# Performance work log

Hardware: AMD Instinct MI355X
Metric: run time of the kernel (lower is better)

The kernel has to match this reference:

```python
import jax, jax.numpy as jnp
import numpy as np

B, N, C, H, K = 16, 1024, 384, 6, 8
HID = int(C * 2.0)  # mlp_ratio = 2.0
HD = C // H


def _layernorm(x, w, b, eps=1e-5):
    m = x.mean(-1, keepdims=True)
    v = ((x - m) ** 2).mean(-1, keepdims=True)
    return (x - m) * jax.lax.rsqrt(v + eps) * w + b


def setup_inputs() -> dict:
    key = jax.random.key(0)
    ks = jax.random.split(key, 16)
    x = jax.random.normal(ks[0], (B, N, C), jnp.float32)
    # knn indices within each batch, offset by batch*N (as in get_knn_index)
    idx = jax.random.randint(ks[1], (B, K, N), 0, N)
    base = jnp.arange(B, dtype=jnp.int32)[:, None, None] * N
    knn_index = (idx + base).reshape(-1).astype(jnp.int32)
    s = 0.02
    p = {
        "x": x,
        "knn_index": knn_index,
        "ln1_w": jnp.ones((C,), jnp.float32),
        "ln1_b": jnp.zeros((C,), jnp.float32),
        "w_qkv": jax.random.normal(ks[2], (C, 3 * C), jnp.float32) * s,  # qkv_bias=False
        "w_proj": jax.random.normal(ks[3], (C, C), jnp.float32) * s,
        "b_proj": jnp.zeros((C,), jnp.float32),
        "w_knn": jax.random.normal(ks[4], (2 * C, C), jnp.float32) * s,
        "b_knn": jnp.zeros((C,), jnp.float32),
        "w_merge": jax.random.normal(ks[5], (2 * C, C), jnp.float32) * s,
        "b_merge": jnp.zeros((C,), jnp.float32),
        "ln2_w": jnp.ones((C,), jnp.float32),
        "ln2_b": jnp.zeros((C,), jnp.float32),
        "w_fc1": jax.random.normal(ks[6], (C, HID), jnp.float32) * s,
        "b_fc1": jnp.zeros((HID,), jnp.float32),
        "w_fc2": jax.random.normal(ks[7], (HID, C), jnp.float32) * s,
        "b_fc2": jnp.zeros((C,), jnp.float32),
    }
    return p


def reference(x, knn_index, ln1_w, ln1_b, w_qkv, w_proj, b_proj, w_knn, b_knn,
              w_merge, b_merge, ln2_w, ln2_b, w_fc1, b_fc1, w_fc2, b_fc2):
    nx = _layernorm(x, ln1_w, ln1_b)  # [B,N,C]

    # --- self attention ---
    qkv = (nx @ w_qkv).reshape(B, N, 3, H, HD)
    q, k, v = qkv[:, :, 0], qkv[:, :, 1], qkv[:, :, 2]  # [B,N,H,HD]
    scale = HD ** (-0.5)
    attn = jnp.einsum("bnhd,bmhd->bhnm", q, k) * scale
    attn = jax.nn.softmax(attn, axis=-1)
    a_out = jnp.einsum("bhnm,bmhd->bnhd", attn, v).reshape(B, N, C)
    x1 = a_out @ w_proj + b_proj

    # --- graph feature: gather, relative concat, Linear+LeakyReLU, max over k ---
    feat = nx.reshape(B * N, C)[knn_index].reshape(B, K, N, C)
    center = nx[:, None, :, :]  # [B,1,N,C]
    g = jnp.concatenate([feat - center, jnp.broadcast_to(center, (B, K, N, C))], axis=-1)
    knn_f = jax.nn.leaky_relu(g @ w_knn + b_knn, negative_slope=0.2)
    knn_f = knn_f.max(axis=1)  # [B,N,C]

    x1 = jnp.concatenate([x1, knn_f], axis=-1) @ w_merge + b_merge
    x = x + x1

    # --- MLP ---
    h = _layernorm(x, ln2_w, ln2_b)
    h = jax.nn.gelu(h @ w_fc1 + b_fc1, approximate=False) @ w_fc2 + b_fc2
    return x + h
```

## Files before the change

### kernel.cpp

```cpp
#include <hip/hip_runtime.h>
#include <hip/hip_bf16.h>
#include <math.h>

#define BN_ROWS 16384
#define CDIM 384
#define NH 6
#define BBATCH 16
#define NNN 1024

typedef unsigned short u16;
typedef unsigned int u32;
typedef __attribute__((ext_vector_type(8))) short short8;
typedef __attribute__((ext_vector_type(4))) float floatx4;

__device__ __forceinline__ float b2f(u16 s) { return __uint_as_float(((u32)s) << 16); }
__device__ __forceinline__ u16 f2b(float f) {
    __hip_bfloat16 h = __float2bfloat16(f);
    u16 s; __builtin_memcpy(&s, &h, 2); return s;
}
__device__ __forceinline__ u32 cvt_pk_bf16(float lo, float hi) {
    u32 r;
    asm("v_cvt_pk_bf16_f32 %0, %1, %2" : "=v"(r) : "v"(lo), "v"(hi));
    return r;
}
__device__ __forceinline__ void gload_lds16(const u16* g, u16* l) {
    __builtin_amdgcn_global_load_lds(
        (const __attribute__((address_space(1))) unsigned int*)g,
        (__attribute__((address_space(3))) unsigned int*)l, 16, 0, 0);
}

__global__ __launch_bounds__(256) void pack_all(
    const float* __restrict__ W0, u16* __restrict__ T0,
    const float* __restrict__ W1, u16* __restrict__ T1,
    const float* __restrict__ W2, u16* __restrict__ T2,
    const float* __restrict__ W3, u16* __restrict__ T3,
    const float* __restrict__ W4, u16* __restrict__ T4,
    const float* __restrict__ W5, u16* __restrict__ T5)
{
    const float* W; u16* T; int K, N;
    switch (blockIdx.z) {
        case 0: W = W0; T = T0; K = 384; N = 1152; break;
        case 1: W = W1; T = T1; K = 384; N = 384;  break;
        case 2: W = W2; T = T2; K = 768; N = 384;  break;
        case 3: W = W3; T = T3; K = 768; N = 384;  break;
        case 4: W = W4; T = T4; K = 384; N = 768;  break;
        default: W = W5; T = T5; K = 768; N = 384; break;
    }
    const int n0 = blockIdx.x * 32, k0 = blockIdx.y * 32;
    if (n0 >= N || k0 >= K) return;
    __shared__ float s[32][33];
    const int tx = threadIdx.x & 31, ty = threadIdx.x >> 5;
#pragma unroll
    for (int i = 0; i < 4; ++i)
        s[ty + 8 * i][tx] = W[(size_t)(k0 + ty + 8 * i) * N + n0 + tx];
    __syncthreads();
#pragma unroll
    for (int i = 0; i < 4; ++i)
        T[(size_t)(n0 + ty + 8 * i) * K + k0 + tx] = f2b(s[tx][ty + 8 * i]);
}

__global__ __launch_bounds__(64) void ln_kernel(const float* __restrict__ xin,
                                                const float* __restrict__ w,
                                                const float* __restrict__ b,
                                                u16* __restrict__ out)
{
    const int row = blockIdx.x;
    const int t = threadIdx.x;
    const size_t base = (size_t)row * CDIM;
    float v[6];
#pragma unroll
    for (int i = 0; i < 6; ++i) v[i] = xin[base + t + 64 * i];
    float s = 0.f, s2 = 0.f;
#pragma unroll
    for (int i = 0; i < 6; ++i) { s += v[i]; s2 += v[i] * v[i]; }
#pragma unroll
    for (int m = 1; m < 64; m <<= 1) {
        s  += __shfl_xor(s,  m, 64);
        s2 += __shfl_xor(s2, m, 64);
    }
    const float mean = s * (1.0f / CDIM);
    const float var  = s2 * (1.0f / CDIM) - mean * mean;
    const float rs   = rsqrtf(var + 1e-5f);
#pragma unroll
    for (int i = 0; i < 6; ++i) {
        int c = t + 64 * i;
        out[base + c] = f2b((v[i] - mean) * rs * w[c] + b[c]);
    }
}

template<int ACT, bool HAS_BIAS, bool HAS_RES, bool OUT_F32, int MODE, int NT, bool SWZ>
__global__ __launch_bounds__(256) void gemm_mfma_kernel(
    const u16* __restrict__ A, int lda,
    const u16* __restrict__ Bt, const u16* __restrict__ Bt2, int ldbt,
    u16* Cb, u16* Cb2, float* Cf, int ldc,
    const float* __restrict__ bias,
    const float* res,
    int K)
{
    constexpr int NTL = NT / 32;
    __shared__ u16 As[3][128 * 32];
    __shared__ u16 Bs[3][NT * 32];
    const int tid  = threadIdx.x;
    const int wv   = tid >> 6;
    const int lane = tid & 63;
    const int l15  = lane & 15;
    const int quad = lane >> 4;

    int m0, n0;
    if (SWZ) {
        const int nbx = gridDim.x;
        const int total = nbx * gridDim.y;
        int lin = blockIdx.x + nbx * blockIdx.y;
        const int cpx = total >> 3;
        lin = (lin & 7) * cpx + (lin >> 3);
        m0 = (lin / nbx) * 128;
        n0 = (lin % nbx) * NT;
    } else {
        m0 = blockIdx.y * 128;
        n0 = blockIdx.x * NT;
    }

    const int woffm = (wv >> 1) * 64;
    const int woffn = (wv & 1) * (NT / 2);

    const u16* bsrc = (MODE == 2 && n0 >= 384) ? Bt2 : Bt;
    const int  bn0  = (MODE == 2 && n0 >= 384) ? (n0 - 384) : n0;

    floatx4 acc[4][NTL];
#pragma unroll
    for (int mt = 0; mt < 4; ++mt)
#pragma unroll
        for (int nt = 0; nt < NTL; ++nt) acc[mt][nt] = (floatx4){0.f, 0.f, 0.f, 0.f};

    const int gsw  = 8 * ((lane & 3) ^ ((lane >> 3) & 3));
    const int rloc = lane >> 2;
    const int rdsw = 8 * (quad ^ ((l15 >> 1) & 3));

    auto stage = [&](int kt, int p) {
#pragma unroll
        for (int j = 0; j < 2; ++j) {
            const int slab = 32 * wv + 16 * j;
            gload_lds16(A + (size_t)(m0 + slab + rloc) * lda + kt + gsw, &As[p][slab * 32]);
        }
        if (NT == 128) {
#pragma unroll
            for (int j = 0; j < 2; ++j) {
                const int slab = 32 * wv + 16 * j;
                gload_lds16(bsrc + (size_t)(bn0 + slab + rloc) * ldbt + kt + gsw, &Bs[p][slab * 32]);
            }
        } else {
            const int slab = 16 * wv;
            gload_lds16(bsrc + (size_t)(bn0 + slab + rloc) * ldbt + kt + gsw, &Bs[p][slab * 32]);
        }
    };

    stage(0, 0);
    if (32 < K) stage(32, 1);
    int s = 0;
    for (int kt = 0; kt < K; kt += 32, ++s) {
        if (kt + 32 < K) {
            if constexpr (NT == 128) asm volatile("s_waitcnt vmcnt(4)" ::: "memory");
            else                     asm volatile("s_waitcnt vmcnt(3)" ::: "memory");
        } else {
            asm volatile("s_waitcnt vmcnt(0)" ::: "memory");
        }
        __builtin_amdgcn_sched_barrier(0);
        __builtin_amdgcn_s_barrier();
        __builtin_amdgcn_sched_barrier(0);

        const u16* Ac = As[s % 3];
        const u16* Bc = Bs[s % 3];
        short8 af[4], bf[NTL];
#pragma unroll
        for (int mt = 0; mt < 4; ++mt)
            af[mt] = *(const short8*)(Ac + (woffm + mt * 16 + l15) * 32 + rdsw);
#pragma unroll
        for (int nt = 0; nt < NTL; ++nt)
            bf[nt] = *(const short8*)(Bc + (woffn + nt * 16 + l15) * 32 + rdsw);
#pragma unroll
        for (int mt = 0; mt < 4; ++mt)
#pragma unroll
            for (int nt = 0; nt < NTL; ++nt)
                acc[mt][nt] = __builtin_amdgcn_mfma_f32_16x16x32_bf16(
                    bf[nt], af[mt], acc[mt][nt], 0, 0, 0);
        if (kt + 64 < K) stage(kt + 64, (s + 2) % 3);
    }

#pragma unroll
    for (int mt = 0; mt < 4; ++mt) {
        const int gr = m0 + woffm + mt * 16 + l15;
#pragma unroll
        for (int nt = 0; nt < NTL; ++nt) {
            const int gc0 = n0 + woffn + nt * 16 + quad * 4;
            float v4[4];
#pragma unroll
            for (int rr = 0; rr < 4; ++rr) v4[rr] = acc[mt][nt][rr];
            if (HAS_BIAS) {
                const floatx4 bv = *(const floatx4*)(bias + gc0);
#pragma unroll
                for (int rr = 0; rr < 4; ++rr) v4[rr] += bv[rr];
            }
            if (MODE == 2) {
                if (gc0 >= 384) {
                    const floatx4 bv = *(const floatx4*)(bias + gc0 - 384);
#pragma unroll
                    for (int rr = 0; rr < 4; ++rr) v4[rr] += bv[rr];
                }
            }
            if (ACT == 1) {
#pragma unroll
                for (int rr = 0; rr < 4; ++rr)
                    v4[rr] = 0.5f * v4[rr] * (1.0f + erff(v4[rr] * 0.70710678118654752f));
            }
            if (HAS_RES) {
                const floatx4 rv = *(const floatx4*)(res + (size_t)gr * ldc + gc0);
#pragma unroll
                for (int rr = 0; rr < 4; ++rr) v4[rr] += rv[rr];
            }
            if (MODE == 1) {
                const int t3  = gc0 / 384;
                const int rem = gc0 - t3 * 384;
                const int hh = rem >> 6, dd = rem & 63;
                const int bb = gr >> 10, nn = gr & 1023;
                u32 lo = cvt_pk_bf16(v4[0], v4[1]);
                u32 hi = cvt_pk_bf16(v4[2], v4[3]);
                *(uint2*)(Cb + ((size_t)((bb * 6 + hh) * 1024 + nn)) * 192 + t3 * 64 + dd) =
                    make_uint2(lo, hi);
            } else if (MODE == 2) {
                u32 lo = cvt_pk_bf16(v4[0], v4[1]);
                u32 hi = cvt_pk_bf16(v4[2], v4[3]);
                if (gc0 < 384)
                    *(uint2*)(Cb  + (size_t)gr * 384 + gc0)       = make_uint2(lo, hi);
                else
                    *(uint2*)(Cb2 + (size_t)gr * 384 + gc0 - 384) = make_uint2(lo, hi);
            } else if (OUT_F32) {
                floatx4 vv = {v4[0], v4[1], v4[2], v4[3]};
                *(floatx4*)(Cf + (size_t)gr * ldc + gc0) = vv;
            } else {
                u32 lo = cvt_pk_bf16(v4[0], v4[1]);
                u32 hi = cvt_pk_bf16(v4[2], v4[3]);
                *(uint2*)(Cb + (size_t)gr * ldc + gc0) = make_uint2(lo, hi);
            }
        }
    }
}

__global__ __launch_bounds__(256) void attn_mfma_kernel(const u16* __restrict__ qkv2,
                                                        u16* __restrict__ aout)
{
    const int id = blockIdx.x;
    const int rxcd = id & 7;
    const int j = id >> 3;
    const int slab = rxcd + 8 * (j % 12);
    const int qtile = j / 12;
    const int b = slab / NH, h = slab % NH;

    const int wave = threadIdx.x >> 6;
    const int lane = threadIdx.x & 63;
    const int l15 = lane & 15;
    const int quad = lane >> 4;
    const int qbase = qtile * 128 + wave * 32;
    const int tid = threadIdx.x;

    const u16* slabp = qkv2 + ((size_t)(b * NH + h) << 10) * 192;

    __shared__ __align__(16) u16 Ks[64 * 72];
    __shared__ __align__(16) u16 Vt[64 * 72];
    __shared__ __align__(16) u16 Ps[4][32 * 72];

    short8 qf[2][2];
#pragma unroll
    for (int nt = 0; nt < 2; ++nt) {
        const u16* qrow = slabp + (size_t)(qbase + nt * 16 + l15) * 192;
        qf[nt][0] = *(const short8*)(qrow + quad * 8);
        qf[nt][1] = *(const short8*)(qrow + 32 + quad * 8);
    }

    short8 vones;
#pragma unroll
    for (int i = 0; i < 8; ++i) vones[i] = (l15 == 0) ? (short)0x3F80 : (short)0;

    floatx4 Oacc[2][4];
    floatx4 rAcc[2];
#pragma unroll
    for (int mt = 0; mt < 2; ++mt) {
        rAcc[mt] = (floatx4){0.f, 0.f, 0.f, 0.f};
#pragma unroll
        for (int nt = 0; nt < 4; ++nt) Oacc[mt][nt] = (floatx4){0.f, 0.f, 0.f, 0.f};
    }

    const int key = tid >> 2, dblk = (tid & 3) * 16;
    const int kp2 = tid & 31, db = (tid >> 5) * 8;
    uint4 kr0, kr1, vr0, vr1;
    {
        const u16* kp = slabp + (size_t)key * 192 + 64 + dblk;
        kr0 = *(const uint4*)(kp);
        kr1 = *(const uint4*)(kp + 8);
        const u16* vp = slabp + (size_t)(2 * kp2) * 192 + 128 + db;
        vr0 = *(const uint4*)(vp);
        vr1 = *(const uint4*)(vp + 192);
    }

    for (int kc = 0; kc < NNN; kc += 64) {
        *(uint4*)(Ks + key * 72 + dblk)     = kr0;
        *(uint4*)(Ks + key * 72 + dblk + 8) = kr1;
        {
            u32 a0[4] = {vr0.x, vr0.y, vr0.z, vr0.w};
            u32 a1[4] = {vr1.x, vr1.y, vr1.z, vr1.w};
#pragma unroll
            for (int i = 0; i < 4; ++i) {
                u32 lo = __builtin_amdgcn_perm(a1[i], a0[i], 0x05040100u);
                u32 hi = __builtin_amdgcn_perm(a1[i], a0[i], 0x07060302u);
                *(u32*)(Vt + (size_t)(db + 2 * i)     * 72 + 2 * kp2) = lo;
                *(u32*)(Vt + (size_t)(db + 2 * i + 1) * 72 + 2 * kp2) = hi;
            }
        }
        __syncthreads();

        if (kc + 64 < NNN) {
            const u16* kp = slabp + (size_t)(kc + 64 + key) * 192 + 64 + dblk;
            kr0 = *(const uint4*)(kp);
            kr1 = *(const uint4*)(kp + 8);
            const u16* vp = slabp + (size_t)(kc + 64 + 2 * kp2) * 192 + 128 + db;
            vr0 = *(const uint4*)(vp);
            vr1 = *(const uint4*)(vp + 192);
        }

        floatx4 sc[4][2];
        __builtin_amdgcn_s_setprio(1);
#pragma unroll
        for (int kt_ = 0; kt_ < 4; ++kt_) {
            short8 kf0 = *(const short8*)(Ks + (kt_ * 16 + l15) * 72 + quad * 8);
            short8 kf1 = *(const short8*)(Ks + (kt_ * 16 + l15) * 72 + 32 + quad * 8);
#pragma unroll
            for (int nt = 0; nt < 2; ++nt) {
                floatx4 s = {0.f, 0.f, 0.f, 0.f};
                s = __builtin_amdgcn_mfma_f32_16x16x32_bf16(kf0, qf[nt][0], s, 0, 0, 0);
                s = __builtin_amdgcn_mfma_f32_16x16x32_bf16(kf1, qf[nt][1], s, 0, 0, 0);
                sc[kt_][nt] = s;
            }
        }
        __builtin_amdgcn_s_setprio(0);

#pragma unroll
        for (int kt_ = 0; kt_ < 4; ++kt_)
#pragma unroll
            for (int nt = 0; nt < 2; ++nt) {
                float pv[4];
#pragma unroll
                for (int rr = 0; rr < 4; ++rr)
                    pv[rr] = __expf(sc[kt_][nt][rr] * 0.125f);
                u32 lo = cvt_pk_bf16(pv[0], pv[1]);
                u32 hi = cvt_pk_bf16(pv[2], pv[3]);
                *(uint2*)(Ps[wave] + (nt * 16 + l15) * 72 + kt_ * 16 + quad * 4) =
                    make_uint2(lo, hi);
            }

        short8 pf[2][2];
#pragma unroll
        for (int mt = 0; mt < 2; ++mt) {
            pf[mt][0] = *(const short8*)(Ps[wave] + (mt * 16 + l15) * 72 + quad * 8);
            pf[mt][1] = *(const short8*)(Ps[wave] + (mt * 16 + l15) * 72 + 32 + quad * 8);
        }
        __builtin_amdgcn_s_setprio(1);
#pragma unroll
        for (int mt = 0; mt < 2; ++mt) {
            rAcc[mt] = __builtin_amdgcn_mfma_f32_16x16x32_bf16(pf[mt][0], vones, rAcc[mt], 0, 0, 0);
            rAcc[mt] = __builtin_amdgcn_mfma_f32_16x16x32_bf16(pf[mt][1], vones, rAcc[mt], 0, 0, 0);
        }
#pragma unroll
        for (int nt = 0; nt < 4; ++nt) {
#pragma unroll
            for (int kk = 0; kk < 2; ++kk) {
                short8 vf = *(const short8*)(Vt + (size_t)(nt * 16 + l15) * 72 + kk * 32 + quad * 8);
#pragma unroll
                for (int mt = 0; mt < 2; ++mt)
                    Oacc[mt][nt] = __builtin_amdgcn_mfma_f32_16x16x32_bf16(
                        pf[mt][kk], vf, Oacc[mt][nt], 0, 0, 0);
            }
        }
        __builtin_amdgcn_s_setprio(0);
        __syncthreads();
    }

#pragma unroll
    for (int mt = 0; mt < 2; ++mt) {
#pragma unroll
        for (int rr = 0; rr < 4; ++rr) {
            float l = __shfl(rAcc[mt][rr], quad << 4, 64);
            float inv = 1.0f / l;
            int q = qbase + mt * 16 + quad * 4 + rr;
#pragma unroll
            for (int nt = 0; nt < 4; ++nt)
                aout[(size_t)(b * NNN + q) * CDIM + h * 64 + nt * 16 + l15] =
                    f2b(Oacc[mt][nt][rr] * inv);
        }
    }
}

__global__ __launch_bounds__(128) void knnmax_kernel(const u16* __restrict__ t1,
                                                     const u16* __restrict__ t2,
                                                     const int* __restrict__ idx,
                                                     u16* __restrict__ x1cat)
{
    const int bn = blockIdx.x * 2 + (threadIdx.x >> 6);
    const int lane = threadIdx.x & 63;
    if (lane >= 48) return;
    const int b = bn >> 10, n = bn & 1023;
    int ind[8];
#pragma unroll
    for (int k = 0; k < 8; ++k) ind[k] = idx[b * 8192 + k * 1024 + n];
    const int c0 = lane * 8;
    const size_t rbase = (size_t)bn * CDIM + c0;
    short8 v1 = *(const short8*)(t1 + rbase);
    short8 v2 = *(const short8*)(t2 + rbase);
    float basef[8], mx[8];
#pragma unroll
    for (int j = 0; j < 8; ++j) {
        basef[j] = b2f((u16)v2[j]) - b2f((u16)v1[j]);
        mx[j] = -1e30f;
    }
#pragma unroll
    for (int k = 0; k < 8; ++k) {
        short8 nv = *(const short8*)(t1 + (size_t)ind[k] * CDIM + c0);
#pragma unroll
        for (int j = 0; j < 8; ++j) {
            float v = b2f((u16)nv[j]) + basef[j];
            v = (v > 0.f) ? v : 0.2f * v;
            mx[j] = fmaxf(mx[j], v);
        }
    }
    short8 ov;
#pragma unroll
    for (int j = 0; j < 8; ++j) ov[j] = (short)f2b(mx[j]);
    *(short8*)(x1cat + (size_t)bn * 768 + CDIM + c0) = ov;
}

extern "C" void kernel_launch(void* const* d_in, const int* in_sizes, int n_in,
                              void* d_out, int out_size, void* d_ws, size_t ws_size,
                              hipStream_t stream)
{
    (void)in_sizes; (void)n_in; (void)out_size; (void)ws_size;
    const float* x     = (const float*)d_in[0];
    const int*   knn   = (const int*)d_in[1];
    const float* ln1w  = (const float*)d_in[2];
    const float* ln1b  = (const float*)d_in[3];
    const float* wqkv  = (const float*)d_in[4];
    const float* wproj = (const float*)d_in[5];
    const float* bproj = (const float*)d_in[6];
    const float* wknn  = (const float*)d_in[7];
    const float* bknn  = (const float*)d_in[8];
    const float* wmrg  = (const float*)d_in[9];
    const float* bmrg  = (const float*)d_in[10];
    const float* ln2w  = (const float*)d_in[11];
    const float* ln2b  = (const float*)d_in[12];
    const float* wfc1  = (const float*)d_in[13];
    const float* bfc1  = (const float*)d_in[14];
    const float* wfc2  = (const float*)d_in[15];
    const float* bfc2  = (const float*)d_in[16];

    u16* wsb = (u16*)d_ws;
    const size_t RE = (size_t)BN_ROWS * CDIM;
    u16* nxb   = wsb;
    u16* qkvb  = wsb + RE;
    u16* x1cat = wsb + RE;
    u16* t1b   = wsb + 3 * RE;
    u16* hinb  = wsb;
    u16* h1b   = wsb + RE;
    u16* wqkvT  = wsb + 4 * RE;
    u16* wprojT = wqkvT + 442368;
    u16* wknnT  = wprojT + 147456;
    u16* wmrgT  = wknnT + 294912;
    u16* wfc1T  = wmrgT + 294912;
    u16* wfc2T  = wfc1T + 294912;
    u16*   aoutb = (u16*)d_out;
    u16*   t2b   = (u16*)d_out;
    float* xmid  = (float*)d_out;

    pack_all<<<dim3(36, 24, 6), 256, 0, stream>>>(
        wqkv, wqkvT, wproj, wprojT, wknn, wknnT, wmrg, wmrgT, wfc1, wfc1T, wfc2, wfc2T);
    ln_kernel<<<BN_ROWS, 64, 0, stream>>>(x, ln1w, ln1b, nxb);
    gemm_mfma_kernel<0, false, false, false, 1, 128, true><<<dim3(9, 128), 256, 0, stream>>>(
        nxb, CDIM, wqkvT, nullptr, CDIM, qkvb, nullptr, nullptr, 0, nullptr, nullptr, CDIM);
    attn_mfma_kernel<<<768, 256, 0, stream>>>(qkvb, aoutb);
    gemm_mfma_kernel<0, true, false, false, 0, 64, true><<<dim3(6, 128), 256, 0, stream>>>(
        aoutb, CDIM, wprojT, nullptr, CDIM, x1cat, nullptr, nullptr, 768, bproj, nullptr, CDIM);
    gemm_mfma_kernel<0, false, false, false, 2, 128, true><<<dim3(6, 128), 256, 0, stream>>>(
        nxb, CDIM, wknnT, wknnT + 384, 768, t1b, t2b, nullptr, CDIM, bknn, nullptr, CDIM);
    knnmax_kernel<<<BN_ROWS / 2, 128, 0, stream>>>(t1b, t2b, knn, x1cat);
    gemm_mfma_kernel<0, true, true, true, 0, 64, true><<<dim3(6, 128), 256, 0, stream>>>(
        x1cat, 768, wmrgT, nullptr, 768, nullptr, nullptr, xmid, CDIM, bmrg, x, 768);
    ln_kernel<<<BN_ROWS, 64, 0, stream>>>(xmid, ln2w, ln2b, hinb);
    gemm_mfma_kernel<1, true, false, false, 0, 128, true><<<dim3(6, 128), 256, 0, stream>>>(
        hinb, CDIM, wfc1T, nullptr, CDIM, h1b, nullptr, nullptr, 768, bfc1, nullptr, CDIM);
    gemm_mfma_kernel<0, true, true, true, 0, 64, true><<<dim3(6, 128), 256, 0, stream>>>(
        h1b, 768, wfc2T, nullptr, 768, nullptr, nullptr, (float*)d_out, CDIM, bfc2, xmid, 768);
}
```

Before: 309.4 us.

## Fuse QKV and KNN projection GEMMs into one launch with double-buffered LDS

Adds a MODE 3 path to the GEMM so the QKV projection and both halves of the KNN linear run as one wider launch over nx (15 column tiles). This removes a kernel launch and reads nx once instead of twice. The GEMM pipeline also drops from triple to double buffering, with an extra barrier per k-step, which cuts LDS use but shortens prefetch depth. Workspace buffers are moved so t1/t2 live in the output buffer and aout in the workspace.

```diff
diff --git a/kernel.cpp b/kernel.cpp
--- a/kernel.cpp
+++ b/kernel.cpp
@@ -92,14 +92,14 @@
 __global__ __launch_bounds__(256) void gemm_mfma_kernel(
     const u16* __restrict__ A, int lda,
     const u16* __restrict__ Bt, const u16* __restrict__ Bt2, int ldbt,
-    u16* Cb, u16* Cb2, float* Cf, int ldc,
+    u16* Cb, u16* Cb2, u16* Cb3, float* Cf, int ldc,
     const float* __restrict__ bias,
     const float* res,
     int K)
 {
     constexpr int NTL = NT / 32;
-    __shared__ u16 As[3][128 * 32];
-    __shared__ u16 Bs[3][NT * 32];
+    __shared__ u16 As[2][128 * 32];
+    __shared__ u16 Bs[2][NT * 32];
     const int tid  = threadIdx.x;
     const int wv   = tid >> 6;
     const int lane = tid & 63;
@@ -123,8 +123,16 @@
     const int woffm = (wv >> 1) * 64;
     const int woffn = (wv & 1) * (NT / 2);
 
-    const u16* bsrc = (MODE == 2 && n0 >= 384) ? Bt2 : Bt;
-    const int  bn0  = (MODE == 2 && n0 >= 384) ? (n0 - 384) : n0;
+    const u16* bsrc; int brow0, koff, bld;
+    if constexpr (MODE == 3) {
+        if (n0 < 1152)      { bsrc = Bt;  brow0 = n0;        koff = 0;   bld = 384; }
+        else if (n0 < 1536) { bsrc = Bt2; brow0 = n0 - 1152; koff = 0;   bld = 768; }
+        else                { bsrc = Bt2; brow0 = n0 - 1536; koff = 384; bld = 768; }
+    } else {
+        bsrc  = (MODE == 2 && n0 >= 384) ? Bt2 : Bt;
+        brow0 = (MODE == 2 && n0 >= 384) ? (n0 - 384) : n0;
+        koff = 0; bld = ldbt;
+    }
 
     floatx4 acc[4][NTL];
 #pragma unroll
@@ -146,18 +154,20 @@
 #pragma unroll
             for (int j = 0; j < 2; ++j) {
                 const int slab = 32 * wv + 16 * j;
-                gload_lds16(bsrc + (size_t)(bn0 + slab + rloc) * ldbt + kt + gsw, &Bs[p][slab * 32]);
+                gload_lds16(bsrc + (size_t)(brow0 + slab + rloc) * bld + koff + kt + gsw,
+                            &Bs[p][slab * 32]);
             }
         } else {
             const int slab = 16 * wv;
-            gload_lds16(bsrc + (size_t)(bn0 + slab + rloc) * ldbt + kt + gsw, &Bs[p][slab * 32]);
+            gload_lds16(bsrc + (size_t)(brow0 + slab + rloc) * bld + koff + kt + gsw,
+                        &Bs[p][slab * 32]);
         }
     };
 
     stage(0, 0);
-    if (32 < K) stage(32, 1);
-    int s = 0;
-    for (int kt = 0; kt < K; kt += 32, ++s) {
+    stage(32, 1);
+    int cur = 0;
+    for (int kt = 0; kt < K; kt += 32) {
         if (kt + 32 < K) {
             if constexpr (NT == 128) asm volatile("s_waitcnt vmcnt(4)" ::: "memory");
             else                     asm volatile("s_waitcnt vmcnt(3)" ::: "memory");
@@ -168,22 +178,24 @@
         __builtin_amdgcn_s_barrier();
         __builtin_amdgcn_sched_barrier(0);
 
-        const u16* Ac = As[s % 3];
-        const u16* Bc = Bs[s % 3];
         short8 af[4], bf[NTL];
 #pragma unroll
         for (int mt = 0; mt < 4; ++mt)
-            af[mt] = *(const short8*)(Ac + (woffm + mt * 16 + l15) * 32 + rdsw);
+            af[mt] = *(const short8*)(As[cur] + (woffm + mt * 16 + l15) * 32 + rdsw);
 #pragma unroll
         for (int nt = 0; nt < NTL; ++nt)
-            bf[nt] = *(const short8*)(Bc + (woffn + nt * 16 + l15) * 32 + rdsw);
+            bf[nt] = *(const short8*)(Bs[cur] + (woffn + nt * 16 + l15) * 32 + rdsw);
 #pragma unroll
         for (int mt = 0; mt < 4; ++mt)
 #pragma unroll
             for (int nt = 0; nt < NTL; ++nt)
                 acc[mt][nt] = __builtin_amdgcn_mfma_f32_16x16x32_bf16(
                     bf[nt], af[mt], acc[mt][nt], 0, 0, 0);
-        if (kt + 64 < K) stage(kt + 64, (s + 2) % 3);
+        __builtin_amdgcn_sched_barrier(0);
+        __builtin_amdgcn_s_barrier();
+        __builtin_amdgcn_sched_barrier(0);
+        if (kt + 64 < K) stage(kt + 64, cur);
+        cur ^= 1;
     }
 
 #pragma unroll
@@ -200,12 +212,15 @@
 #pragma unroll
                 for (int rr = 0; rr < 4; ++rr) v4[rr] += bv[rr];
             }
-            if (MODE == 2) {
-                if (gc0 >= 384) {
-                    const floatx4 bv = *(const floatx4*)(bias + gc0 - 384);
-#pragma unroll
-                    for (int rr = 0; rr < 4; ++rr) v4[rr] += bv[rr];
-                }
+            if (MODE == 2 && gc0 >= 384) {
+                const floatx4 bv = *(const floatx4*)(bias + gc0 - 384);
+#pragma unroll
+                for (int rr = 0; rr < 4; ++rr) v4[rr] += bv[rr];
+            }
+            if (MODE == 3 && gc0 >= 1536) {
+                const floatx4 bv = *(const floatx4*)(bias + gc0 - 1536);
+#pragma unroll
+                for (int rr = 0; rr < 4; ++rr) v4[rr] += bv[rr];
             }
             if (ACT == 1) {
 #pragma unroll
@@ -217,7 +232,7 @@
 #pragma unroll
                 for (int rr = 0; rr < 4; ++rr) v4[rr] += rv[rr];
             }
-            if (MODE == 1) {
+            if (MODE == 1 || (MODE == 3 && gc0 < 1152)) {
                 const int t3  = gc0 / 384;
                 const int rem = gc0 - t3 * 384;
                 const int hh = rem >> 6, dd = rem & 63;
@@ -226,6 +241,13 @@
                 u32 hi = cvt_pk_bf16(v4[2], v4[3]);
                 *(uint2*)(Cb + ((size_t)((bb * 6 + hh) * 1024 + nn)) * 192 + t3 * 64 + dd) =
                     make_uint2(lo, hi);
+            } else if (MODE == 3) {
+                u32 lo = cvt_pk_bf16(v4[0], v4[1]);
+                u32 hi = cvt_pk_bf16(v4[2], v4[3]);
+                if (gc0 < 1536)
+                    *(uint2*)(Cb2 + (size_t)gr * 384 + gc0 - 1152) = make_uint2(lo, hi);
+                else
+                    *(uint2*)(Cb3 + (size_t)gr * 384 + gc0 - 1536) = make_uint2(lo, hi);
             } else if (MODE == 2) {
                 u32 lo = cvt_pk_bf16(v4[0], v4[1]);
                 u32 hi = cvt_pk_bf16(v4[2], v4[3]);
@@ -463,36 +485,34 @@
     const size_t RE = (size_t)BN_ROWS * CDIM;
     u16* nxb   = wsb;
     u16* qkvb  = wsb + RE;
+    u16* aoutb = wsb;
     u16* x1cat = wsb + RE;
-    u16* t1b   = wsb + 3 * RE;
     u16* hinb  = wsb;
     u16* h1b   = wsb + RE;
+    u16* t1b   = (u16*)d_out;
+    u16* t2b   = (u16*)d_out + RE;
+    float* xmid = (float*)d_out;
     u16* wqkvT  = wsb + 4 * RE;
     u16* wprojT = wqkvT + 442368;
     u16* wknnT  = wprojT + 147456;
     u16* wmrgT  = wknnT + 294912;
     u16* wfc1T  = wmrgT + 294912;
     u16* wfc2T  = wfc1T + 294912;
-    u16*   aoutb = (u16*)d_out;
-    u16*   t2b   = (u16*)d_out;
-    float* xmid  = (float*)d_out;
 
     pack_all<<<dim3(36, 24, 6), 256, 0, stream>>>(
         wqkv, wqkvT, wproj, wprojT, wknn, wknnT, wmrg, wmrgT, wfc1, wfc1T, wfc2, wfc2T);
     ln_kernel<<<BN_ROWS, 64, 0, stream>>>(x, ln1w, ln1b, nxb);
-    gemm_mfma_kernel<0, false, false, false, 1, 128, true><<<dim3(9, 128), 256, 0, stream>>>(
-        nxb, CDIM, wqkvT, nullptr, CDIM, qkvb, nullptr, nullptr, 0, nullptr, nullptr, CDIM);
+    gemm_mfma_kernel<0, false, false, false, 3, 128, true><<<dim3(15, 128), 256, 0, stream>>>(
+        nxb, CDIM, wqkvT, wknnT, 384, qkvb, t1b, t2b, nullptr, 0, bknn, nullptr, CDIM);
     attn_mfma_kernel<<<768, 256, 0, stream>>>(qkvb, aoutb);
     gemm_mfma_kernel<0, true, false, false, 0, 64, true><<<dim3(6, 128), 256, 0, stream>>>(
-        aoutb, CDIM, wprojT, nullptr, CDIM, x1cat, nullptr, nullptr, 768, bproj, nullptr, CDIM);
-    gemm_mfma_kernel<0, false, false, false, 2, 128, true><<<dim3(6, 128), 256, 0, stream>>>(
-        nxb, CDIM, wknnT, wknnT + 384, 768, t1b, t2b, nullptr, CDIM, bknn, nullptr, CDIM);
+        aoutb, CDIM, wprojT, nullptr, CDIM, x1cat, nullptr, nullptr, nullptr, 768, bproj, nullptr, CDIM);
     knnmax_kernel<<<BN_ROWS / 2, 128, 0, stream>>>(t1b, t2b, knn, x1cat);
     gemm_mfma_kernel<0, true, true, true, 0, 64, true><<<dim3(6, 128), 256, 0, stream>>>(
-        x1cat, 768, wmrgT, nullptr, 768, nullptr, nullptr, xmid, CDIM, bmrg, x, 768);
+        x1cat, 768, wmrgT, nullptr, 768, nullptr, nullptr, nullptr, xmid, CDIM, bmrg, x, 768);
     ln_kernel<<<BN_ROWS, 64, 0, stream>>>(xmid, ln2w, ln2b, hinb);
     gemm_mfma_kernel<1, true, false, false, 0, 128, true><<<dim3(6, 128), 256, 0, stream>>>(
-        hinb, CDIM, wfc1T, nullptr, CDIM, h1b, nullptr, nullptr, 768, bfc1, nullptr, CDIM);
+        hinb, CDIM, wfc1T, nullptr, CDIM, h1b, nullptr, nullptr, nullptr, 768, bfc1, nullptr, CDIM);
     gemm_mfma_kernel<0, true, true, true, 0, 64, true><<<dim3(6, 128), 256, 0, stream>>>(
-        h1b, 768, wfc2T, nullptr, 768, nullptr, nullptr, (float*)d_out, CDIM, bfc2, xmid, 768);
-}
+        h1b, 768, wfc2T, nullptr, 768, nullptr, nullptr, nullptr, (float*)d_out, CDIM, bfc2, xmid, 768);
+}
```

New measurement: 306.1 us. About the same (-1.1%).
